# Kernel optimization log

Hardware: AMD Instinct MI355X
Metric: run time of the kernel (lower is better)

The kernel has to match this reference:

```python
import jax, jax.numpy as jnp
import numpy as np

NUM_HEADS = 16
HIDDEN = 1024
HEAD_DIM = HIDDEN // NUM_HEADS
BS, SEQ = 2, 2048


def setup_inputs() -> dict:
    key = jax.random.key(0)
    ks = jax.random.split(key, 9)
    s = 1.0 / np.sqrt(HIDDEN)
    return {
        "Q": jax.random.normal(ks[0], (BS, SEQ, HIDDEN), jnp.float32),
        "K": jax.random.normal(ks[1], (BS, SEQ, HIDDEN), jnp.float32),
        "V": jax.random.normal(ks[2], (BS, SEQ, HIDDEN), jnp.float32),
        "attention_mask": jnp.zeros((BS, 1, 1, SEQ), jnp.float32),
        # nn.Linear weights stored as [in, out] (already transposed)
        "Wq": jax.random.uniform(ks[3], (HIDDEN, HIDDEN), jnp.float32, -s, s),
        "bq": jax.random.uniform(ks[4], (HIDDEN,), jnp.float32, -s, s),
        "Wk": jax.random.uniform(ks[5], (HIDDEN, HIDDEN), jnp.float32, -s, s),
        "bk": jax.random.uniform(ks[6], (HIDDEN,), jnp.float32, -s, s),
        "Wv": jax.random.uniform(ks[7], (HIDDEN, HIDDEN), jnp.float32, -s, s),
        "bv": jax.random.uniform(ks[8], (HIDDEN,), jnp.float32, -s, s),
    }


def _split_heads(x):
    b, s, _ = x.shape
    return x.reshape(b, s, NUM_HEADS, HEAD_DIM).transpose(0, 2, 1, 3)  # [b,h,s,d]


def reference(Q, K, V, attention_mask, Wq, bq, Wk, bk, Wv, bv):
    q = _split_heads(Q @ Wq + bq)  # [b,h,s,d]
    k = _split_heads(K @ Wk + bk)
    v = _split_heads(V @ Wv + bv)
    score = jnp.einsum("bhqd,bhkd->bhqk", q, k)
    # NOTE: original adds mask BEFORE scaling by 1/sqrt(d)
    score = (score + attention_mask) / np.sqrt(HEAD_DIM)
    attn = jax.nn.softmax(score, axis=-1)
    out = jnp.einsum("bhqk,bhkd->bqhd", attn, v)  # [b,q,h,d]
    b, s = Q.shape[:2]
    return out.reshape(b, s, NUM_HEADS * HEAD_DIM)
```

## Files before the change

### kernel.cpp

```cpp
#include <hip/hip_runtime.h>
#include <hip/hip_bf16.h>
#include <stdint.h>

#define SEQ    2048
#define HIDDEN 1024
#define NH     16
#define HD     64

#define SC_LOG2E_8 0.18033688011112042f
#define SM_SHIFT   16.0f

typedef __bf16 bf16x8 __attribute__((ext_vector_type(8)));
typedef float  f32x4  __attribute__((ext_vector_type(4)));
typedef float  f32x16 __attribute__((ext_vector_type(16)));
typedef unsigned int uint32x2 __attribute__((ext_vector_type(2)));

typedef __attribute__((address_space(1))) void* as1vp;
typedef __attribute__((address_space(3))) void* as3vp;

__device__ __forceinline__ void gload_lds16(const void* g, void* l) {
  __builtin_amdgcn_global_load_lds((as1vp)(void*)g, (as3vp)l, 16, 0, 0);
}

__device__ __forceinline__ uint16_t f2bf(float f) {
  uint32_t x;
  __builtin_memcpy(&x, &f, 4);
  x += 0x7FFFu + ((x >> 16) & 1u);
  return (uint16_t)(x >> 16);
}

__device__ __forceinline__ uint32_t pkbf(float lo, float hi) {
  union { __bf16 v[2]; uint32_t u; } t;
  t.v[0] = (__bf16)lo; t.v[1] = (__bf16)hi;
  return t.u;
}

__device__ __forceinline__ uint32x2 plswap(uint32_t lo, uint32_t hi) {
  return __builtin_amdgcn_permlane32_swap(lo, hi, false, false);
}

__device__ __forceinline__ float xhalf32(float x, int lane) {
  uint32_t a;
  __builtin_memcpy(&a, &x, 4);
  uint32x2 r = plswap(a, a);
  uint32_t p = (lane < 32) ? r[1] : r[0];
  float f;
  __builtin_memcpy(&f, &p, 4);
  return f;
}

__device__ __forceinline__ float exp2_fast(float x) {
  return __builtin_amdgcn_exp2f(x);
}

__global__ __launch_bounds__(256) void k_prep(
    const float* __restrict__ Q, const float* __restrict__ K, const float* __restrict__ V,
    const float* __restrict__ mask,
    const float* __restrict__ W0, const float* __restrict__ W1, const float* __restrict__ W2,
    uint16_t* __restrict__ Qb, uint16_t* __restrict__ Kb, uint16_t* __restrict__ Vb,
    float* __restrict__ mask_sc,
    uint16_t* __restrict__ T0, uint16_t* __restrict__ T1, uint16_t* __restrict__ T2) {
  __shared__ uint16_t t[64][65];
  if (blockIdx.x > 2048) {
    const int bi = blockIdx.x - 2049;
    const float* W = (blockIdx.y == 0) ? W0 : (blockIdx.y == 1) ? W1 : W2;
    uint16_t*    T = (blockIdx.y == 0) ? T0 : (blockIdx.y == 1) ? T1 : T2;
    const int bx = bi & 15, by = bi >> 4;
    const int tx = threadIdx.x & 63, ty = threadIdx.x >> 6;
    for (int i = ty; i < 64; i += 4)
      t[i][tx] = f2bf(W[(by * 64 + i) * HIDDEN + bx * 64 + tx]);
    __syncthreads();
    for (int i = ty; i < 64; i += 4)
      T[(bx * 64 + i) * HIDDEN + by * 64 + tx] = t[tx][i];
    return;
  }
  if (blockIdx.x == 2048) {
    if (blockIdx.y < 2) {
      const int i = (blockIdx.y * 256 + threadIdx.x) * 8;
      float4 a = *(const float4*)(mask + i);
      float4 b = *(const float4*)(mask + i + 4);
      a.x = a.x * SC_LOG2E_8 - SM_SHIFT; a.y = a.y * SC_LOG2E_8 - SM_SHIFT;
      a.z = a.z * SC_LOG2E_8 - SM_SHIFT; a.w = a.w * SC_LOG2E_8 - SM_SHIFT;
      b.x = b.x * SC_LOG2E_8 - SM_SHIFT; b.y = b.y * SC_LOG2E_8 - SM_SHIFT;
      b.z = b.z * SC_LOG2E_8 - SM_SHIFT; b.w = b.w * SC_LOG2E_8 - SM_SHIFT;
      *(float4*)(mask_sc + i) = a;
      *(float4*)(mask_sc + i + 4) = b;
    }
    return;
  }
  const float* src = (blockIdx.y == 0) ? Q : (blockIdx.y == 1) ? K : V;
  uint16_t*    dst = (blockIdx.y == 0) ? Qb : (blockIdx.y == 1) ? Kb : Vb;
  const int i = (blockIdx.x * 256 + threadIdx.x) * 8;
  float4 v0 = *(const float4*)(src + i);
  float4 v1 = *(const float4*)(src + i + 4);
  uint16_t tmp[8];
  tmp[0] = f2bf(v0.x); tmp[1] = f2bf(v0.y); tmp[2] = f2bf(v0.z); tmp[3] = f2bf(v0.w);
  tmp[4] = f2bf(v1.x); tmp[5] = f2bf(v1.y); tmp[6] = f2bf(v1.z); tmp[7] = f2bf(v1.w);
  __builtin_memcpy(dst + i, tmp, 16);
}

__global__ __launch_bounds__(256) void k_qkv_gemm(
    const uint16_t* __restrict__ Qb, const uint16_t* __restrict__ Kb, const uint16_t* __restrict__ Vb,
    const uint16_t* __restrict__ WTq, const uint16_t* __restrict__ WTk, const uint16_t* __restrict__ WTv,
    const float* __restrict__ Bq, const float* __restrict__ Bk, const float* __restrict__ Bv,
    uint16_t* __restrict__ q_ws, uint16_t* __restrict__ k_ws, uint16_t* __restrict__ v_ws) {
  const int wg  = blockIdx.x;
  const int swz = (wg & 7) * 192 + (wg >> 3);
  const int mode = swz >> 9;
  const int rem  = swz & 511;
  const int m0   = (rem >> 4) * 128;
  const int n0   = (rem & 15) * 64;

  const uint16_t* X   = (mode == 0) ? Qb : (mode == 1) ? Kb : Vb;
  const uint16_t* WT  = (mode == 0) ? WTq : (mode == 1) ? WTk : WTv;
  const float*    bia = (mode == 0) ? Bq  : (mode == 1) ? Bk  : Bv;

  __shared__ uint16_t As[128 * 64];
  __shared__ uint16_t Bs[64 * 64];
  char* AsB = (char*)As;
  char* BsB = (char*)Bs;

  const int tid  = threadIdx.x;
  const int lane = tid & 63;
  const int w    = tid >> 6;
  const int wr   = w >> 1, wc = w & 1;

  const int lrow   = lane >> 3;
  const int srccol = ((lane & 7) * 16) ^ (lrow << 4);

  f32x4 acc[4][2];
  const f32x4 zero = {0.f, 0.f, 0.f, 0.f};
#pragma unroll
  for (int i = 0; i < 4; ++i)
#pragma unroll
    for (int j = 0; j < 2; ++j) acc[i][j] = zero;

  const char* Ab = (const char*)X;
  const char* Bb = (const char*)WT;

  for (int kt = 0; kt < 16; ++kt) {
    __syncthreads();
    const int kbyte = kt * 128;
#pragma unroll
    for (int i = 0; i < 4; ++i) {
      const int r = w * 32 + i * 8;
      gload_lds16(Ab + (size_t)(m0 + r + lrow) * (HIDDEN * 2) + kbyte + srccol, AsB + r * 128);
    }
#pragma unroll
    for (int i = 0; i < 2; ++i) {
      const int r = w * 16 + i * 8;
      gload_lds16(Bb + (size_t)(n0 + r + lrow) * (HIDDEN * 2) + kbyte + srccol, BsB + r * 128);
    }
    __syncthreads();
#pragma unroll
    for (int kc = 0; kc < 2; ++kc) {
      const int chunk = kc * 64 + (lane >> 4) * 16;
      bf16x8 a[4], b[2];
#pragma unroll
      for (int f = 0; f < 4; ++f) {
        const int ra = wr * 64 + f * 16 + (lane & 15);
        a[f] = *(const bf16x8*)(AsB + ra * 128 + (chunk ^ ((ra & 7) << 4)));
      }
#pragma unroll
      for (int f = 0; f < 2; ++f) {
        const int rb = wc * 32 + f * 16 + (lane & 15);
        b[f] = *(const bf16x8*)(BsB + rb * 128 + (chunk ^ ((rb & 7) << 4)));
      }
#pragma unroll
      for (int fm = 0; fm < 4; ++fm)
#pragma unroll
        for (int fn = 0; fn < 2; ++fn)
          acc[fm][fn] = __builtin_amdgcn_mfma_f32_16x16x32_bf16(a[fm], b[fn], acc[fm][fn], 0, 0, 0);
    }
  }

  float bfrag[2];
#pragma unroll
  for (int fn = 0; fn < 2; ++fn)
    bfrag[fn] = bia[n0 + wc * 32 + fn * 16 + (lane & 15)];

#pragma unroll
  for (int fm = 0; fm < 4; ++fm) {
    const int mrow0 = m0 + wr * 64 + fm * 16 + (lane >> 4) * 4;
    const int b0 = mrow0 >> 11;
    const int sq = mrow0 & (SEQ - 1);
#pragma unroll
    for (int fn = 0; fn < 2; ++fn) {
      const int n = n0 + wc * 32 + fn * 16 + (lane & 15);
      const int h = n >> 6, d = n & 63;
      const size_t bh = (size_t)(b0 * NH + h);
      if (mode == 2) {
        const int kt2 = sq >> 6, ks = (sq >> 4) & 3, hv = (sq >> 3) & 1, jj = sq & 7;
        const int dt = d >> 5, lnv = hv * 32 + (d & 31);
        uint16_t tmp[4];
#pragma unroll
        for (int j = 0; j < 4; ++j) tmp[j] = f2bf(acc[fm][fn][j] + bfrag[fn]);
        __builtin_memcpy(v_ws + ((((bh * 32 + kt2) * 2 + dt) * 4 + ks) * 64 + lnv) * 8 + jj,
                         tmp, 8);
      } else if (mode == 1) {
        const int kt2 = sq >> 6, c = (sq >> 5) & 1, ql = sq & 31;
        const int slot = d >> 4, hk = (d >> 3) & 1, jk = d & 7;
        uint16_t* base = k_ws + ((((bh * 32 + kt2) * 2 + c) * 4 + slot) * 64 + hk * 32 + ql) * 8 + jk;
#pragma unroll
        for (int j = 0; j < 4; ++j) base[j * 8] = f2bf(acc[fm][fn][j] + bfrag[fn]);
      } else {
        const int qt32 = sq >> 5, ql = sq & 31;
        const int slot = d >> 4, hq = (d >> 3) & 1, jq = d & 7;
        uint16_t* base = q_ws + (((bh * 64 + qt32) * 4 + slot) * 64 + hq * 32 + ql) * 8 + jq;
#pragma unroll
        for (int j = 0; j < 4; ++j)
          base[j * 8] = f2bf((acc[fm][fn][j] + bfrag[fn]) * SC_LOG2E_8);
      }
    }
  }
}

__global__ __launch_bounds__(256) void k_attn(
    const uint16_t* __restrict__ q_ws, const uint16_t* __restrict__ k_ws,
    const uint16_t* __restrict__ v_ws, const float* __restrict__ mask_sc,
    float* __restrict__ out) {
  __shared__ float smem[3][64][33];

  const int tid = threadIdx.x, lane = tid & 63, w = tid >> 6;
  const int wg  = blockIdx.x;
  const int swz = (wg & 7) * 256 + (wg >> 3);
  const int bh  = swz >> 6;
  const int qt  = swz & 63;
  const int b   = bh >> 4;
  const int h   = bh & 15;
  const int q0  = qt * 32;
  const int ql  = lane & 31;
  const int hi  = lane >> 5;

  const char* qfb = (const char*)q_ws + ((size_t)bh * 64 + qt) * 4096;
  const char* kfb = (const char*)k_ws + (size_t)bh * 262144 + lane * 16;
  const char* vfb = (const char*)v_ws + (size_t)bh * 262144 + lane * 16;
  const float* mrow = mask_sc + b * SEQ;

  bf16x8 qB[4];
#pragma unroll
  for (int s = 0; s < 4; ++s)
    qB[s] = *(const bf16x8*)(qfb + s * 1024 + lane * 16);

  const f32x16 zero16 = {0.f};
  f32x16 Oacc[2];
  Oacc[0] = zero16; Oacc[1] = zero16;
  float lpart = 0.f;

  const int kbeg = w * 8, kend = kbeg + 8;

  for (int kt = kbeg; kt < kend; ++kt) {
    const char* kt_k = kfb + (size_t)kt * 8192;
    const char* kt_v = vfb + (size_t)kt * 8192;

    bf16x8 kf[8];
#pragma unroll
    for (int i = 0; i < 8; ++i) kf[i] = *(const bf16x8*)(kt_k + i * 1024);

    f32x16 P0, P1;
#pragma unroll
    for (int g = 0; g < 4; ++g) {
      f32x4 mk0 = *(const f32x4*)(mrow + kt * 64 + g * 8 + 4 * hi);
      f32x4 mk1 = *(const f32x4*)(mrow + kt * 64 + 32 + g * 8 + 4 * hi);
#pragma unroll
      for (int t = 0; t < 4; ++t) { P0[g * 4 + t] = mk0[t]; P1[g * 4 + t] = mk1[t]; }
    }

    __builtin_amdgcn_s_setprio(1);
#pragma unroll
    for (int s = 0; s < 4; ++s)
      P0 = __builtin_amdgcn_mfma_f32_32x32x16_bf16(kf[s], qB[s], P0, 0, 0, 0);
#pragma unroll
    for (int s = 0; s < 4; ++s)
      P1 = __builtin_amdgcn_mfma_f32_32x32x16_bf16(kf[4 + s], qB[s], P1, 0, 0, 0);
    __builtin_amdgcn_s_setprio(0);

    bf16x8 vA[8];
#pragma unroll
    for (int i = 0; i < 8; ++i) vA[i] = *(const bf16x8*)(kt_v + i * 1024);

    float s0 = 0.f, s1 = 0.f, s2a = 0.f, s3 = 0.f;
#pragma unroll
    for (int r = 0; r < 16; r += 4) {
      P0[r]     = exp2_fast(P0[r]);      s0  += P0[r];
      P0[r + 1] = exp2_fast(P0[r + 1]);  s1  += P0[r + 1];
      P0[r + 2] = exp2_fast(P0[r + 2]);  s2a += P0[r + 2];
      P0[r + 3] = exp2_fast(P0[r + 3]);  s3  += P0[r + 3];
      P1[r]     = exp2_fast(P1[r]);      s0  += P1[r];
      P1[r + 1] = exp2_fast(P1[r + 1]);  s1  += P1[r + 1];
      P1[r + 2] = exp2_fast(P1[r + 2]);  s2a += P1[r + 2];
      P1[r + 3] = exp2_fast(P1[r + 3]);  s3  += P1[r + 3];
    }
    lpart += (s0 + s1) + (s2a + s3);

    bf16x8 pb[4];
#pragma unroll
    for (int ks = 0; ks < 4; ++ks) {
      const int o = (ks & 1) * 8;
      uint32_t w0, w1, w2, w3;
      if (ks < 2) {
        w0 = pkbf(P0[o + 0], P0[o + 1]);
        w1 = pkbf(P0[o + 2], P0[o + 3]);
        w2 = pkbf(P0[o + 4], P0[o + 5]);
        w3 = pkbf(P0[o + 6], P0[o + 7]);
      } else {
        w0 = pkbf(P1[o + 0], P1[o + 1]);
        w1 = pkbf(P1[o + 2], P1[o + 3]);
        w2 = pkbf(P1[o + 4], P1[o + 5]);
        w3 = pkbf(P1[o + 6], P1[o + 7]);
      }
      uint32x2 r02 = plswap(w0, w2);
      uint32x2 r13 = plswap(w1, w3);
      uint32_t wv[4] = {r02[0], r13[0], r02[1], r13[1]};
      __builtin_memcpy(&pb[ks], wv, 16);
    }

    __builtin_amdgcn_s_setprio(1);
#pragma unroll
    for (int ks = 0; ks < 4; ++ks) {
      Oacc[0] = __builtin_amdgcn_mfma_f32_32x32x16_bf16(vA[ks],     pb[ks], Oacc[0], 0, 0, 0);
      Oacc[1] = __builtin_amdgcn_mfma_f32_32x32x16_bf16(vA[4 + ks], pb[ks], Oacc[1], 0, 0, 0);
    }
    __builtin_amdgcn_s_setprio(0);
  }

  if (w > 0) {
    float* s = smem[w - 1][lane];
#pragma unroll
    for (int r = 0; r < 16; ++r) { s[r] = Oacc[0][r]; s[16 + r] = Oacc[1][r]; }
    s[32] = lpart;
  }
  __syncthreads();
  if (w > 0) return;

#pragma unroll
  for (int p = 0; p < 3; ++p) {
    const float* s = smem[p][lane];
#pragma unroll
    for (int r = 0; r < 16; ++r) { Oacc[0][r] += s[r]; Oacc[1][r] += s[16 + r]; }
    lpart += s[32];
  }

  const float ltot = lpart + xhalf32(lpart, lane);
  const float linv = 1.f / ltot;
  float* orow = out + ((size_t)(b * SEQ) + q0 + ql) * HIDDEN + h * HD;
#pragma unroll
  for (int dt = 0; dt < 2; ++dt)
#pragma unroll
    for (int g = 0; g < 4; ++g) {
      f32x4 o;
#pragma unroll
      for (int t = 0; t < 4; ++t) o[t] = Oacc[dt][g * 4 + t] * linv;
      *(f32x4*)(orow + dt * 32 + g * 8 + 4 * hi) = o;
    }
}

extern "C" void kernel_launch(void* const* d_in, const int* in_sizes, int n_in,
                              void* d_out, int out_size, void* d_ws, size_t ws_size,
                              hipStream_t stream) {
  (void)in_sizes; (void)n_in; (void)out_size; (void)ws_size;
  const float* Q    = (const float*)d_in[0];
  const float* K    = (const float*)d_in[1];
  const float* V    = (const float*)d_in[2];
  const float* mask = (const float*)d_in[3];
  const float* Wq   = (const float*)d_in[4];
  const float* bq   = (const float*)d_in[5];
  const float* Wk   = (const float*)d_in[6];
  const float* bk   = (const float*)d_in[7];
  const float* Wv   = (const float*)d_in[8];
  const float* bv   = (const float*)d_in[9];

  uint16_t* ws   = (uint16_t*)d_ws;
  uint16_t* wt_q = ws;
  uint16_t* wt_k = wt_q + HIDDEN * HIDDEN;
  uint16_t* wt_v = wt_k + HIDDEN * HIDDEN;
  const size_t qkv = (size_t)2 * SEQ * HIDDEN;
  uint16_t* Qb   = wt_v + HIDDEN * HIDDEN;
  uint16_t* Kb   = Qb + qkv;
  uint16_t* Vb   = Kb + qkv;
  uint16_t* q_ws = Vb + qkv;
  uint16_t* k_ws = q_ws + qkv;
  uint16_t* v_ws = k_ws + qkv;
  float* mask_sc = (float*)(v_ws + qkv);

  k_prep<<<dim3(2305, 3), 256, 0, stream>>>(Q, K, V, mask, Wq, Wk, Wv,
                                            Qb, Kb, Vb, mask_sc,
                                            wt_q, wt_k, wt_v);
  k_qkv_gemm<<<dim3(1536), 256, 0, stream>>>(
      Qb, Kb, Vb, wt_q, wt_k, wt_v, bq, bk, bv, q_ws, k_ws, v_ws);
  k_attn<<<dim3(2048), 256, 0, stream>>>(q_ws, k_ws, v_ws, mask_sc,
                                         (float*)d_out);
}
```

Before: 111.7 us.

## Process two 32-row query tiles per attention block to reuse K/V loads

```diff
diff --git a/kernel.cpp b/kernel.cpp
--- a/kernel.cpp
+++ b/kernel.cpp
@@ -215,37 +215,38 @@
   }
 }
 
-__global__ __launch_bounds__(256) void k_attn(
+__global__ __launch_bounds__(256, 1) void k_attn(
     const uint16_t* __restrict__ q_ws, const uint16_t* __restrict__ k_ws,
     const uint16_t* __restrict__ v_ws, const float* __restrict__ mask_sc,
     float* __restrict__ out) {
-  __shared__ float smem[3][64][33];
+  __shared__ float smem[3][64][67];
 
   const int tid = threadIdx.x, lane = tid & 63, w = tid >> 6;
   const int wg  = blockIdx.x;
-  const int swz = (wg & 7) * 256 + (wg >> 3);
-  const int bh  = swz >> 6;
-  const int qt  = swz & 63;
+  const int swz = (wg & 7) * 128 + (wg >> 3);
+  const int bh  = swz >> 5;
+  const int qt  = swz & 31;
   const int b   = bh >> 4;
   const int h   = bh & 15;
-  const int q0  = qt * 32;
+  const int q0  = qt * 64;
   const int ql  = lane & 31;
   const int hi  = lane >> 5;
 
-  const char* qfb = (const char*)q_ws + ((size_t)bh * 64 + qt) * 4096;
+  const char* qfb = (const char*)q_ws + ((size_t)bh * 64 + qt * 2) * 4096;
   const char* kfb = (const char*)k_ws + (size_t)bh * 262144 + lane * 16;
   const char* vfb = (const char*)v_ws + (size_t)bh * 262144 + lane * 16;
   const float* mrow = mask_sc + b * SEQ;
 
-  bf16x8 qB[4];
-#pragma unroll
-  for (int s = 0; s < 4; ++s)
-    qB[s] = *(const bf16x8*)(qfb + s * 1024 + lane * 16);
+  bf16x8 qBa[4], qBb[4];
+#pragma unroll
+  for (int s = 0; s < 4; ++s) {
+    qBa[s] = *(const bf16x8*)(qfb + s * 1024 + lane * 16);
+    qBb[s] = *(const bf16x8*)(qfb + 4096 + s * 1024 + lane * 16);
+  }
 
   const f32x16 zero16 = {0.f};
-  f32x16 Oacc[2];
-  Oacc[0] = zero16; Oacc[1] = zero16;
-  float lpart = 0.f;
+  f32x16 Oa0 = zero16, Oa1 = zero16, Ob0 = zero16, Ob1 = zero16;
+  float la = 0.f, lb = 0.f;
 
   const int kbeg = w * 8, kend = kbeg + 8;
 
@@ -257,69 +258,123 @@
 #pragma unroll
     for (int i = 0; i < 8; ++i) kf[i] = *(const bf16x8*)(kt_k + i * 1024);
 
-    f32x16 P0, P1;
+    f32x4 mk0[4], mk1[4];
 #pragma unroll
     for (int g = 0; g < 4; ++g) {
-      f32x4 mk0 = *(const f32x4*)(mrow + kt * 64 + g * 8 + 4 * hi);
-      f32x4 mk1 = *(const f32x4*)(mrow + kt * 64 + 32 + g * 8 + 4 * hi);
-#pragma unroll
-      for (int t = 0; t < 4; ++t) { P0[g * 4 + t] = mk0[t]; P1[g * 4 + t] = mk1[t]; }
-    }
+      mk0[g] = *(const f32x4*)(mrow + kt * 64 + g * 8 + 4 * hi);
+      mk1[g] = *(const f32x4*)(mrow + kt * 64 + 32 + g * 8 + 4 * hi);
+    }
+
+    bf16x8 pba[4], pbb[4];
+
+    {
+      f32x16 P0, P1;
+#pragma unroll
+      for (int g = 0; g < 4; ++g)
+#pragma unroll
+        for (int t = 0; t < 4; ++t) { P0[g * 4 + t] = mk0[g][t]; P1[g * 4 + t] = mk1[g][t]; }
+      __builtin_amdgcn_s_setprio(1);
+#pragma unroll
+      for (int s = 0; s < 4; ++s)
+        P0 = __builtin_amdgcn_mfma_f32_32x32x16_bf16(kf[s], qBa[s], P0, 0, 0, 0);
+#pragma unroll
+      for (int s = 0; s < 4; ++s)
+        P1 = __builtin_amdgcn_mfma_f32_32x32x16_bf16(kf[4 + s], qBa[s], P1, 0, 0, 0);
+      __builtin_amdgcn_s_setprio(0);
+
+      float s0 = 0.f, s1 = 0.f, s2a = 0.f, s3 = 0.f;
+#pragma unroll
+      for (int r = 0; r < 16; r += 4) {
+        P0[r]     = exp2_fast(P0[r]);      s0  += P0[r];
+        P0[r + 1] = exp2_fast(P0[r + 1]);  s1  += P0[r + 1];
+        P0[r + 2] = exp2_fast(P0[r + 2]);  s2a += P0[r + 2];
+        P0[r + 3] = exp2_fast(P0[r + 3]);  s3  += P0[r + 3];
+        P1[r]     = exp2_fast(P1[r]);      s0  += P1[r];
+        P1[r + 1] = exp2_fast(P1[r + 1]);  s1  += P1[r + 1];
+        P1[r + 2] = exp2_fast(P1[r + 2]);  s2a += P1[r + 2];
+        P1[r + 3] = exp2_fast(P1[r + 3]);  s3  += P1[r + 3];
+      }
+      la += (s0 + s1) + (s2a + s3);
+
+#pragma unroll
+      for (int ks = 0; ks < 4; ++ks) {
+        const int o = (ks & 1) * 8;
+        uint32_t w0, w1, w2, w3;
+        if (ks < 2) {
+          w0 = pkbf(P0[o + 0], P0[o + 1]); w1 = pkbf(P0[o + 2], P0[o + 3]);
+          w2 = pkbf(P0[o + 4], P0[o + 5]); w3 = pkbf(P0[o + 6], P0[o + 7]);
+        } else {
+          w0 = pkbf(P1[o + 0], P1[o + 1]); w1 = pkbf(P1[o + 2], P1[o + 3]);
+          w2 = pkbf(P1[o + 4], P1[o + 5]); w3 = pkbf(P1[o + 6], P1[o + 7]);
+        }
+        uint32x2 r02 = plswap(w0, w2);
+        uint32x2 r13 = plswap(w1, w3);
+        uint32_t wv[4] = {r02[0], r13[0], r02[1], r13[1]};
+        __builtin_memcpy(&pba[ks], wv, 16);
+      }
+    }
+
+    {
+      f32x16 P0, P1;
+#pragma unroll
+      for (int g = 0; g < 4; ++g)
+#pragma unroll
+        for (int t = 0; t < 4; ++t) { P0[g * 4 + t] = mk0[g][t]; P1[g * 4 + t] = mk1[g][t]; }
+      __builtin_amdgcn_s_setprio(1);
+#pragma unroll
+      for (int s = 0; s < 4; ++s)
+        P0 = __builtin_amdgcn_mfma_f32_32x32x16_bf16(kf[s], qBb[s], P0, 0, 0, 0);
+#pragma unroll
+      for (int s = 0; s < 4; ++s)
+        P1 = __builtin_amdgcn_mfma_f32_32x32x16_bf16(kf[4 + s], qBb[s], P1, 0, 0, 0);
+      __builtin_amdgcn_s_setprio(0);
+
+      float s0 = 0.f, s1 = 0.f, s2a = 0.f, s3 = 0.f;
+#pragma unroll
+      for (int r = 0; r < 16; r += 4) {
+        P0[r]     = exp2_fast(P0[r]);      s0  += P0[r];
+        P0[r + 1] = exp2_fast(P0[r + 1]);  s1  += P0[r + 1];
+        P0[r + 2] = exp2_fast(P0[r + 2]);  s2a += P0[r + 2];
+        P0[r + 3] = exp2_fast(P0[r + 3]);  s3  += P0[r + 3];
+        P1[r]     = exp2_fast(P1[r]);      s0  += P1[r];
+        P1[r + 1] = exp2_fast(P1[r + 1]);  s1  += P1[r + 1];
+        P1[r + 2] = exp2_fast(P1[r + 2]);  s2a += P1[r + 2];
+        P1[r + 3] = exp2_fast(P1[r + 3]);  s3  += P1[r + 3];
+      }
+      lb += (s0 + s1) + (s2a + s3);
+
+#pragma unroll
+      for (int ks = 0; ks < 4; ++ks) {
+        const int o = (ks & 1) * 8;
+        uint32_t w0, w1, w2, w3;
+        if (ks < 2) {
+          w0 = pkbf(P0[o + 0], P0[o + 1]); w1 = pkbf(P0[o + 2], P0[o + 3]);
+          w2 = pkbf(P0[o + 4], P0[o + 5]); w3 = pkbf(P0[o + 6], P0[o + 7]);
+        } else {
+          w0 = pkbf(P1[o + 0], P1[o + 1]); w1 = pkbf(P1[o + 2], P1[o + 3]);
+          w2 = pkbf(P1[o + 4], P1[o + 5]); w3 = pkbf(P1[o + 6], P1[o + 7]);
+        }
+        uint32x2 r02 = plswap(w0, w2);
+        uint32x2 r13 = plswap(w1, w3);
+        uint32_t wv[4] = {r02[0], r13[0], r02[1], r13[1]};
+        __builtin_memcpy(&pbb[ks], wv, 16);
+      }
+    }
+
+    bf16x8 vA[8];
+#pragma unroll
+    for (int i = 0; i < 8; ++i) vA[i] = *(const bf16x8*)(kt_v + i * 1024);
 
     __builtin_amdgcn_s_setprio(1);
 #pragma unroll
-    for (int s = 0; s < 4; ++s)
-      P0 = __builtin_amdgcn_mfma_f32_32x32x16_bf16(kf[s], qB[s], P0, 0, 0, 0);
-#pragma unroll
-    for (int s = 0; s < 4; ++s)
-      P1 = __builtin_amdgcn_mfma_f32_32x32x16_bf16(kf[4 + s], qB[s], P1, 0, 0, 0);
-    __builtin_amdgcn_s_setprio(0);
-
-    bf16x8 vA[8];
-#pragma unroll
-    for (int i = 0; i < 8; ++i) vA[i] = *(const bf16x8*)(kt_v + i * 1024);
-
-    float s0 = 0.f, s1 = 0.f, s2a = 0.f, s3 = 0.f;
-#pragma unroll
-    for (int r = 0; r < 16; r += 4) {
-      P0[r]     = exp2_fast(P0[r]);      s0  += P0[r];
-      P0[r + 1] = exp2_fast(P0[r + 1]);  s1  += P0[r + 1];
-      P0[r + 2] = exp2_fast(P0[r + 2]);  s2a += P0[r + 2];
-      P0[r + 3] = exp2_fast(P0[r + 3]);  s3  += P0[r + 3];
-      P1[r]     = exp2_fast(P1[r]);      s0  += P1[r];
-      P1[r + 1] = exp2_fast(P1[r + 1]);  s1  += P1[r + 1];
-      P1[r + 2] = exp2_fast(P1[r + 2]);  s2a += P1[r + 2];
-      P1[r + 3] = exp2_fast(P1[r + 3]);  s3  += P1[r + 3];
-    }
-    lpart += (s0 + s1) + (s2a + s3);
-
-    bf16x8 pb[4];
-#pragma unroll
     for (int ks = 0; ks < 4; ++ks) {
-      const int o = (ks & 1) * 8;
-      uint32_t w0, w1, w2, w3;
-      if (ks < 2) {
-        w0 = pkbf(P0[o + 0], P0[o + 1]);
-        w1 = pkbf(P0[o + 2], P0[o + 3]);
-        w2 = pkbf(P0[o + 4], P0[o + 5]);
-        w3 = pkbf(P0[o + 6], P0[o + 7]);
-      } else {
-        w0 = pkbf(P1[o + 0], P1[o + 1]);
-        w1 = pkbf(P1[o + 2], P1[o + 3]);
-        w2 = pkbf(P1[o + 4], P1[o + 5]);
-        w3 = pkbf(P1[o + 6], P1[o + 7]);
-      }
-      uint32x2 r02 = plswap(w0, w2);
-      uint32x2 r13 = plswap(w1, w3);
-      uint32_t wv[4] = {r02[0], r13[0], r02[1], r13[1]};
-      __builtin_memcpy(&pb[ks], wv, 16);
-    }
-
-    __builtin_amdgcn_s_setprio(1);
+      Oa0 = __builtin_amdgcn_mfma_f32_32x32x16_bf16(vA[ks],     pba[ks], Oa0, 0, 0, 0);
+      Oa1 = __builtin_amdgcn_mfma_f32_32x32x16_bf16(vA[4 + ks], pba[ks], Oa1, 0, 0, 0);
+    }
 #pragma unroll
     for (int ks = 0; ks < 4; ++ks) {
-      Oacc[0] = __builtin_amdgcn_mfma_f32_32x32x16_bf16(vA[ks],     pb[ks], Oacc[0], 0, 0, 0);
-      Oacc[1] = __builtin_amdgcn_mfma_f32_32x32x16_bf16(vA[4 + ks], pb[ks], Oacc[1], 0, 0, 0);
+      Ob0 = __builtin_amdgcn_mfma_f32_32x32x16_bf16(vA[ks],     pbb[ks], Ob0, 0, 0, 0);
+      Ob1 = __builtin_amdgcn_mfma_f32_32x32x16_bf16(vA[4 + ks], pbb[ks], Ob1, 0, 0, 0);
     }
     __builtin_amdgcn_s_setprio(0);
   }
@@ -327,8 +382,11 @@
   if (w > 0) {
     float* s = smem[w - 1][lane];
 #pragma unroll
-    for (int r = 0; r < 16; ++r) { s[r] = Oacc[0][r]; s[16 + r] = Oacc[1][r]; }
-    s[32] = lpart;
+    for (int r = 0; r < 16; ++r) {
+      s[r] = Oa0[r]; s[16 + r] = Oa1[r];
+      s[33 + r] = Ob0[r]; s[49 + r] = Ob1[r];
+    }
+    s[32] = la; s[65] = lb;
   }
   __syncthreads();
   if (w > 0) return;
@@ -337,22 +395,36 @@
   for (int p = 0; p < 3; ++p) {
     const float* s = smem[p][lane];
 #pragma unroll
-    for (int r = 0; r < 16; ++r) { Oacc[0][r] += s[r]; Oacc[1][r] += s[16 + r]; }
-    lpart += s[32];
-  }
-
-  const float ltot = lpart + xhalf32(lpart, lane);
-  const float linv = 1.f / ltot;
-  float* orow = out + ((size_t)(b * SEQ) + q0 + ql) * HIDDEN + h * HD;
-#pragma unroll
-  for (int dt = 0; dt < 2; ++dt)
-#pragma unroll
-    for (int g = 0; g < 4; ++g) {
-      f32x4 o;
-#pragma unroll
-      for (int t = 0; t < 4; ++t) o[t] = Oacc[dt][g * 4 + t] * linv;
-      *(f32x4*)(orow + dt * 32 + g * 8 + 4 * hi) = o;
-    }
+    for (int r = 0; r < 16; ++r) {
+      Oa0[r] += s[r]; Oa1[r] += s[16 + r];
+      Ob0[r] += s[33 + r]; Ob1[r] += s[49 + r];
+    }
+    la += s[32]; lb += s[65];
+  }
+
+  const float lat = la + xhalf32(la, lane);
+  const float lbt = lb + xhalf32(lb, lane);
+  const float lia = 1.f / lat;
+  const float lib = 1.f / lbt;
+
+  float* orowa = out + ((size_t)(b * SEQ) + q0 + ql) * HIDDEN + h * HD;
+  float* orowb = out + ((size_t)(b * SEQ) + q0 + 32 + ql) * HIDDEN + h * HD;
+#pragma unroll
+  for (int g = 0; g < 4; ++g) {
+    f32x4 o;
+#pragma unroll
+    for (int t = 0; t < 4; ++t) o[t] = Oa0[g * 4 + t] * lia;
+    *(f32x4*)(orowa + g * 8 + 4 * hi) = o;
+#pragma unroll
+    for (int t = 0; t < 4; ++t) o[t] = Oa1[g * 4 + t] * lia;
+    *(f32x4*)(orowa + 32 + g * 8 + 4 * hi) = o;
+#pragma unroll
+    for (int t = 0; t < 4; ++t) o[t] = Ob0[g * 4 + t] * lib;
+    *(f32x4*)(orowb + g * 8 + 4 * hi) = o;
+#pragma unroll
+    for (int t = 0; t < 4; ++t) o[t] = Ob1[g * 4 + t] * lib;
+    *(f32x4*)(orowb + 32 + g * 8 + 4 * hi) = o;
+  }
 }
 
 extern "C" void kernel_launch(void* const* d_in, const int* in_sizes, int n_in,
@@ -388,6 +460,6 @@
                                             wt_q, wt_k, wt_v);
   k_qkv_gemm<<<dim3(1536), 256, 0, stream>>>(
       Qb, Kb, Vb, wt_q, wt_k, wt_v, bq, bk, bv, q_ws, k_ws, v_ws);
-  k_attn<<<dim3(2048), 256, 0, stream>>>(q_ws, k_ws, v_ws, mask_sc,
+  k_attn<<<dim3(1024), 256, 0, stream>>>(q_ws, k_ws, v_ws, mask_sc,
                                          (float*)d_out);
 }
```

Result: slower. 117.6 us (+5.2%).
